# Optimization experiments

Measured on AMD Instinct MI355X. Metric: run time of the kernel, lower is better.

Reference implementation:

```python
import jax, jax.numpy as jnp
import numpy as np
from jax import lax

B, CIN, COUT, H, W, K = 32, 256, 256, 56, 56, 3

def setup_inputs() -> dict:
    key = jax.random.key(0)
    k1, k2, k3 = jax.random.split(key, 3)
    inp = jax.random.normal(k1, (B, CIN, H, W), dtype=jnp.float32)
    # kaiming-style init for conv kernel, normal init for bias
    fan_in = CIN * K * K
    kernel = jax.random.normal(k2, (COUT, CIN, K, K), dtype=jnp.float32) * np.float32(np.sqrt(2.0 / fan_in))
    bias = jax.random.normal(k3, (COUT,), dtype=jnp.float32)
    return {"inp": inp, "kernel": kernel, "bias": bias}

def reference(inp, kernel, bias):
    # Equivalent to the crossbar path: im2col 3x3 patches @ stacked [kernel|bias]
    # matrix == standard conv2d(padding=1, stride=1) + bias.
    out = lax.conv_general_dilated(
        inp, kernel,
        window_strides=(1, 1),
        padding=((1, 1), (1, 1)),
        dimension_numbers=("NCHW", "OIHW", "NCHW"),
    )
    return out + bias[None, :, None, None]
```

## Files before the change

kernel.cpp:

```cpp
#include <hip/hip_runtime.h>
#include <hip/hip_bf16.h>


#define BB   32
#define CINC 256
#define COUTC 256
#define HH   56
#define WW   56
#define HP   58
#define WP   58
#define PIX_PER_IMG (HH*WW)
#define NPIX (BB*PIX_PER_IMG)
#define KTOT (9*CINC)
#define KB_STEPS (KTOT/32)

#define XT_ELEMS ((size_t)BB*HP*WP*CINC)
#define XT_BYTES (XT_ELEMS*2)
#define WR_ELEMS ((size_t)COUTC*KTOT)
#define WR_BYTES (WR_ELEMS*2)

#define BM 128
#define BN 128
#define BK 32

using frag_t = __attribute__((ext_vector_type(8))) short;
using f32x4  = __attribute__((ext_vector_type(4))) float;

__device__ __forceinline__ void gload_lds16(const void* gsrc, void* ldst) {
  __builtin_amdgcn_global_load_lds(
      (const __attribute__((address_space(1))) unsigned*)gsrc,
      (__attribute__((address_space(3))) unsigned*)ldst, 16, 0, 0);
}

__global__ void xpose_kernel(const float* __restrict__ inp,
                             __hip_bfloat16* __restrict__ xt) {
  int bid = blockIdx.x;
  int hp = bid % HP;
  int t  = bid / HP;
  int cb = t % 4;
  int b  = t / 4;
  __shared__ __hip_bfloat16 tile[64 * 60];
  int tid = threadIdx.x;
  for (int i = tid; i < 64 * 60; i += 256) tile[i] = __float2bfloat16(0.f);
  __syncthreads();
  int h = hp - 1;
  if (h >= 0 && h < HH) {
    const float* src = inp + ((size_t)(b * CINC + cb * 64) * HH + h) * WW;
    for (int i = tid; i < 64 * WW; i += 256) {
      int ci = i / WW, w = i - ci * WW;
      tile[ci * 60 + (w + 1)] = __float2bfloat16(src[(size_t)ci * HH * WW + w]);
    }
  }
  __syncthreads();
  __hip_bfloat16* dst = xt + ((size_t)(b * HP + hp) * WP) * CINC + cb * 64;
  for (int i = tid; i < WP * 64; i += 256) {
    int wp = i >> 6, ci = i & 63;
    dst[(size_t)wp * CINC + ci] = tile[ci * 60 + wp];
  }
}

__global__ void wprep_kernel(const float* __restrict__ k4,
                             __hip_bfloat16* __restrict__ wr) {
  int i = blockIdx.x * 256 + threadIdx.x;
  if (i >= (int)WR_ELEMS) return;
  int co = i / KTOT;
  int k  = i - co * KTOT;
  int tap = k >> 8;
  int ci  = k & 255;
  wr[i] = __float2bfloat16(k4[(co * CINC + ci) * 9 + tap]);
}

__global__ void conv_mfma(const __hip_bfloat16* __restrict__ xt,
                          const __hip_bfloat16* __restrict__ wr,
                          const float* __restrict__ bias,
                          float* __restrict__ out) {
  __shared__ alignas(16) __hip_bfloat16 Alds[BM * BK];
  __shared__ alignas(16) __hip_bfloat16 Blds[BN * BK];

  const int tid  = threadIdx.x;
  const int lane = tid & 63;
  const int wid  = tid >> 6;
  const int wrm  = wid >> 1;
  const int wcn  = wid & 1;
  const int ntile = blockIdx.x;
  const int co0   = blockIdx.y * BM;

  const int qa0 = wid * 128 + lane;
  const int qa1 = qa0 + 64;
  const char* wr_b = (const char*)wr;
  const char* xt_b = (const char*)xt;

  const size_t a_src0 = ((size_t)(co0 + (qa0 >> 2)) * KTOT + (qa0 & 3) * 8) * 2;
  const size_t a_src1 = ((size_t)(co0 + (qa1 >> 2)) * KTOT + (qa1 & 3) * 8) * 2;

  int pxg0 = ntile * BN + (qa0 >> 2);
  int pxg1 = ntile * BN + (qa1 >> 2);
  int b0 = pxg0 / PIX_PER_IMG, hw0 = pxg0 - b0 * PIX_PER_IMG;
  int b1 = pxg1 / PIX_PER_IMG, hw1 = pxg1 - b1 * PIX_PER_IMG;
  int h0 = hw0 / WW, w0 = hw0 - h0 * WW;
  int h1 = hw1 / WW, w1 = hw1 - h1 * WW;
  const size_t b_src0 = ((((size_t)b0 * HP + h0) * WP + w0) * CINC + (qa0 & 3) * 8) * 2;
  const size_t b_src1 = ((((size_t)b1 * HP + h1) * WP + w1) * CINC + (qa1 & 3) * 8) * 2;

  char* a_dst0 = (char*)Alds + (wid * 2) * 1024;
  char* a_dst1 = (char*)Alds + (wid * 2 + 1) * 1024;
  char* b_dst0 = (char*)Blds + (wid * 2) * 1024;
  char* b_dst1 = (char*)Blds + (wid * 2 + 1) * 1024;

  f32x4 acc[4][4] = {};

  const int g  = lane >> 4;
  const int fr = lane & 15;

  for (int kb = 0; kb < KB_STEPS; ++kb) {
    int tap = kb >> 3;
    int r = tap / 3;
    int s = tap - r * 3;
    int ci0 = (kb & 7) * 32;
    size_t aoff = (size_t)kb * 64;
    size_t boff = ((size_t)(r * WP + s) * CINC + ci0) * 2;

    __syncthreads();
    gload_lds16(wr_b + a_src0 + aoff, a_dst0);
    gload_lds16(wr_b + a_src1 + aoff, a_dst1);
    gload_lds16(xt_b + b_src0 + boff, b_dst0);
    gload_lds16(xt_b + b_src1 + boff, b_dst1);
    __syncthreads();

    frag_t a[4], bf[4];
#pragma unroll
    for (int m = 0; m < 4; ++m) {
      int row = wrm * 64 + m * 16 + fr;
      a[m] = *(const frag_t*)((const char*)Alds + row * 64 + g * 16);
    }
#pragma unroll
    for (int n = 0; n < 4; ++n) {
      int row = wcn * 64 + n * 16 + fr;
      bf[n] = *(const frag_t*)((const char*)Blds + row * 64 + g * 16);
    }
#pragma unroll
    for (int m = 0; m < 4; ++m)
#pragma unroll
      for (int n = 0; n < 4; ++n)
        acc[m][n] = __builtin_amdgcn_mfma_f32_16x16x32_bf16(a[m], bf[n], acc[m][n], 0, 0, 0);
  }

  const int fq = lane >> 4;
  int pb[4], phw[4];
#pragma unroll
  for (int n = 0; n < 4; ++n) {
    int pxg = ntile * BN + wcn * 64 + n * 16 + fr;
    pb[n]  = pxg / PIX_PER_IMG;
    phw[n] = pxg - pb[n] * PIX_PER_IMG;
  }
#pragma unroll
  for (int m = 0; m < 4; ++m) {
#pragma unroll
    for (int rg = 0; rg < 4; ++rg) {
      int co = co0 + wrm * 64 + m * 16 + fq * 4 + rg;
      float bv = bias[co];
#pragma unroll
      for (int n = 0; n < 4; ++n) {
        out[((size_t)pb[n] * COUTC + co) * PIX_PER_IMG + phw[n]] = acc[m][n][rg] + bv;
      }
    }
  }
}

__global__ void conv_direct(const float* __restrict__ inp,
                            const float* __restrict__ kern,
                            const float* __restrict__ bias,
                            float* __restrict__ out) {
  int idx = blockIdx.x * 256 + threadIdx.x;
  if (idx >= BB * COUTC * PIX_PER_IMG) return;
  int w = idx % WW;
  int t = idx / WW;
  int h = t % HH; t /= HH;
  int co = t % COUTC;
  int b  = t / COUTC;
  float acc = bias[co];
  for (int ci = 0; ci < CINC; ++ci)
    for (int r = 0; r < 3; ++r) {
      int hh = h + r - 1;
      if (hh < 0 || hh >= HH) continue;
      for (int s = 0; s < 3; ++s) {
        int ww2 = w + s - 1;
        if (ww2 < 0 || ww2 >= WW) continue;
        acc += inp[((size_t)(b * CINC + ci) * HH + hh) * WW + ww2] *
               kern[(co * CINC + ci) * 9 + r * 3 + s];
      }
    }
  out[idx] = acc;
}

extern "C" void kernel_launch(void* const* d_in, const int* in_sizes, int n_in,
                              void* d_out, int out_size, void* d_ws, size_t ws_size,
                              hipStream_t stream) {
  const float* inp  = (const float*)d_in[0];
  const float* kern = (const float*)d_in[1];
  const float* bias = (const float*)d_in[2];
  float* out = (float*)d_out;

  size_t need = XT_BYTES + WR_BYTES;
  if (ws_size < need) {
    int tot = BB * COUTC * PIX_PER_IMG;
    conv_direct<<<(tot + 255) / 256, 256, 0, stream>>>(inp, kern, bias, out);
    return;
  }

  __hip_bfloat16* xt  = (__hip_bfloat16*)d_ws;
  __hip_bfloat16* wrp = (__hip_bfloat16*)((char*)d_ws + XT_BYTES);

  xpose_kernel<<<BB * 4 * HP, 256, 0, stream>>>(inp, xt);
  wprep_kernel<<<(int)((WR_ELEMS + 255) / 256), 256, 0, stream>>>(kern, wrp);
  conv_mfma<<<dim3(NPIX / BN, COUTC / BM), 256, 0, stream>>>(xt, wrp, bias, out);
}
```

Baseline: 209.2 us.

## Rewrite conv GEMM with 32x32 MFMA, triple-buffered LDS pipeline and swizzle

Replaces the single-buffered 128x128 implicit-GEMM kernel with a 256-output-channel by 128-pixel tile. It uses 32x32x16 bf16 MFMAs, a three-stage LDS ring buffer filled by async global-to-LDS loads issued two steps ahead, and an XOR swizzle of the LDS chunks. The block index is remapped so neighbouring blocks are spread across the pixel range. The aim is to overlap global loads with MFMA work, halve the redundant input loads caused by the two channel tiles, and cut LDS bank conflicts. In exchange it uses more LDS and accumulator registers per block and depends on hand-placed waitcnt and barrier ordering.

```diff
diff --git a/kernel.cpp b/kernel.cpp
--- a/kernel.cpp
+++ b/kernel.cpp
@@ -2,29 +2,27 @@
 #include <hip/hip_bf16.h>
 
 
-#define BB   32
-#define CINC 256
+#define BB    32
+#define CINC  256
 #define COUTC 256
-#define HH   56
-#define WW   56
-#define HP   58
-#define WP   58
-#define PIX_PER_IMG (HH*WW)
-#define NPIX (BB*PIX_PER_IMG)
-#define KTOT (9*CINC)
-#define KB_STEPS (KTOT/32)
-
-#define XT_ELEMS ((size_t)BB*HP*WP*CINC)
-#define XT_BYTES (XT_ELEMS*2)
+#define HH    56
+#define WW    56
+#define HP    58
+#define WP    58
+#define PIX_PER_IMG 3136
+#define NPIX  100352
+#define KTOT  2304
+#define NKT   72
+
+#define XT_BYTES ((size_t)BB*HP*WP*CINC*2)
 #define WR_ELEMS ((size_t)COUTC*KTOT)
 #define WR_BYTES (WR_ELEMS*2)
 
-#define BM 128
-#define BN 128
-#define BK 32
+#define BUF_SZ 24576
+#define B_OFF  16384
 
 using frag_t = __attribute__((ext_vector_type(8))) short;
-using f32x4  = __attribute__((ext_vector_type(4))) float;
+using f32x16 = __attribute__((ext_vector_type(16))) float;
 
 __device__ __forceinline__ void gload_lds16(const void* gsrc, void* ldst) {
   __builtin_amdgcn_global_load_lds(
@@ -70,99 +68,140 @@
   wr[i] = __float2bfloat16(k4[(co * CINC + ci) * 9 + tap]);
 }
 
-__global__ void conv_mfma(const __hip_bfloat16* __restrict__ xt,
-                          const __hip_bfloat16* __restrict__ wr,
-                          const float* __restrict__ bias,
-                          float* __restrict__ out) {
-  __shared__ alignas(16) __hip_bfloat16 Alds[BM * BK];
-  __shared__ alignas(16) __hip_bfloat16 Blds[BN * BK];
+__global__ __launch_bounds__(256, 2) void conv_mfma32(
+    const __hip_bfloat16* __restrict__ xt,
+    const __hip_bfloat16* __restrict__ wr,
+    const float* __restrict__ bias,
+    float* __restrict__ out) {
+  __shared__ alignas(16) char lds[3 * BUF_SZ];
 
   const int tid  = threadIdx.x;
   const int lane = tid & 63;
   const int wid  = tid >> 6;
-  const int wrm  = wid >> 1;
-  const int wcn  = wid & 1;
-  const int ntile = blockIdx.x;
-  const int co0   = blockIdx.y * BM;
-
-  const int qa0 = wid * 128 + lane;
-  const int qa1 = qa0 + 64;
+  const int wm   = wid >> 1;
+  const int wn   = wid & 1;
+  const int l31  = lane & 31;
+  const int lhi  = lane >> 5;
+
+  const int bid   = blockIdx.x;
+  const int ntile = (bid & 7) * 98 + (bid >> 3);
+
   const char* wr_b = (const char*)wr;
   const char* xt_b = (const char*)xt;
 
-  const size_t a_src0 = ((size_t)(co0 + (qa0 >> 2)) * KTOT + (qa0 & 3) * 8) * 2;
-  const size_t a_src1 = ((size_t)(co0 + (qa1 >> 2)) * KTOT + (qa1 & 3) * 8) * 2;
-
-  int pxg0 = ntile * BN + (qa0 >> 2);
-  int pxg1 = ntile * BN + (qa1 >> 2);
-  int b0 = pxg0 / PIX_PER_IMG, hw0 = pxg0 - b0 * PIX_PER_IMG;
-  int b1 = pxg1 / PIX_PER_IMG, hw1 = pxg1 - b1 * PIX_PER_IMG;
-  int h0 = hw0 / WW, w0 = hw0 - h0 * WW;
-  int h1 = hw1 / WW, w1 = hw1 - h1 * WW;
-  const size_t b_src0 = ((((size_t)b0 * HP + h0) * WP + w0) * CINC + (qa0 & 3) * 8) * 2;
-  const size_t b_src1 = ((((size_t)b1 * HP + h1) * WP + w1) * CINC + (qa1 & 3) * 8) * 2;
-
-  char* a_dst0 = (char*)Alds + (wid * 2) * 1024;
-  char* a_dst1 = (char*)Alds + (wid * 2 + 1) * 1024;
-  char* b_dst0 = (char*)Blds + (wid * 2) * 1024;
-  char* b_dst1 = (char*)Blds + (wid * 2 + 1) * 1024;
-
-  f32x4 acc[4][4] = {};
-
-  const int g  = lane >> 4;
-  const int fr = lane & 15;
-
-  for (int kb = 0; kb < KB_STEPS; ++kb) {
-    int tap = kb >> 3;
-    int r = tap / 3;
-    int s = tap - r * 3;
-    int ci0 = (kb & 7) * 32;
-    size_t aoff = (size_t)kb * 64;
-    size_t boff = ((size_t)(r * WP + s) * CINC + ci0) * 2;
-
-    __syncthreads();
-    gload_lds16(wr_b + a_src0 + aoff, a_dst0);
-    gload_lds16(wr_b + a_src1 + aoff, a_dst1);
-    gload_lds16(xt_b + b_src0 + boff, b_dst0);
-    gload_lds16(xt_b + b_src1 + boff, b_dst1);
-    __syncthreads();
-
-    frag_t a[4], bf[4];
-#pragma unroll
-    for (int m = 0; m < 4; ++m) {
-      int row = wrm * 64 + m * 16 + fr;
-      a[m] = *(const frag_t*)((const char*)Alds + row * 64 + g * 16);
-    }
-#pragma unroll
-    for (int n = 0; n < 4; ++n) {
-      int row = wcn * 64 + n * 16 + fr;
-      bf[n] = *(const frag_t*)((const char*)Blds + row * 64 + g * 16);
-    }
-#pragma unroll
-    for (int m = 0; m < 4; ++m)
-#pragma unroll
-      for (int n = 0; n < 4; ++n)
-        acc[m][n] = __builtin_amdgcn_mfma_f32_16x16x32_bf16(a[m], bf[n], acc[m][n], 0, 0, 0);
-  }
-
-  const int fq = lane >> 4;
-  int pb[4], phw[4];
-#pragma unroll
-  for (int n = 0; n < 4; ++n) {
-    int pxg = ntile * BN + wcn * 64 + n * 16 + fr;
+  const int lr = lane >> 2;
+  const int sc = (((lane & 3) ^ (lr & 3)) << 4);
+
+  const char* pA0 = wr_b + (size_t)(wid * 64 +  0 + lr) * (KTOT * 2) + sc;
+  const char* pA1 = wr_b + (size_t)(wid * 64 + 16 + lr) * (KTOT * 2) + sc;
+  const char* pA2 = wr_b + (size_t)(wid * 64 + 32 + lr) * (KTOT * 2) + sc;
+  const char* pA3 = wr_b + (size_t)(wid * 64 + 48 + lr) * (KTOT * 2) + sc;
+
+  auto mkB = [&](int jb) -> const char* {
+    int px = ntile * 128 + (wid * 2 + jb) * 16 + lr;
+    int b  = px / PIX_PER_IMG;
+    int hw = px - b * PIX_PER_IMG;
+    int h = hw / WW, w = hw - h * WW;
+    return xt_b + (size_t)((b * HP + h) * WP + w) * (CINC * 2) + sc;
+  };
+  const char* pB0 = mkB(0);
+  const char* pB1 = mkB(1);
+
+#define STG_A(WB, T2) {                                                    \
+    size_t _ao = (size_t)(T2) * 64;                                        \
+    gload_lds16(pA0 + _ao, lds + (WB)*BUF_SZ + (wid * 4 + 0) * 1024);      \
+    gload_lds16(pA1 + _ao, lds + (WB)*BUF_SZ + (wid * 4 + 1) * 1024);      \
+    gload_lds16(pA2 + _ao, lds + (WB)*BUF_SZ + (wid * 4 + 2) * 1024); }
+
+#define STG_B(WB, T2) {                                                    \
+    int _tap = (T2) >> 3; int _rr = _tap / 3, _ss = _tap - _rr * 3;        \
+    size_t _ao = (size_t)(T2) * 64;                                        \
+    size_t _bo = (size_t)(_rr * WP + _ss) * (CINC * 2)                     \
+               + (size_t)((T2) & 7) * 64;                                  \
+    gload_lds16(pA3 + _ao, lds + (WB)*BUF_SZ + (wid * 4 + 3) * 1024);      \
+    gload_lds16(pB0 + _bo, lds + (WB)*BUF_SZ + B_OFF + (wid*2+0) * 1024);  \
+    gload_lds16(pB1 + _bo, lds + (WB)*BUF_SZ + B_OFF + (wid*2+1) * 1024); }
+
+  const int aoff  = (wm * 128 + l31) * 64;
+  const int boffr = (wn * 64 + l31) * 64;
+  const int ck0   = ((lhi ^ (l31 & 3)) << 4);
+  const int ck1   = (((2 + lhi) ^ (l31 & 3)) << 4);
+
+  frag_t fa0[4], fb0[2], fa1[4], fb1[2];
+  f32x16 acc[4][2] = {};
+
+#define RSL(RB, CK, FA, FB) {                                              \
+    const char* _b = lds + (RB)*BUF_SZ;                                    \
+    _Pragma("unroll") for (int m = 0; m < 4; ++m)                          \
+      FA[m] = *(const frag_t*)(_b + aoff + m * 2048 + (CK));               \
+    _Pragma("unroll") for (int n = 0; n < 2; ++n)                          \
+      FB[n] = *(const frag_t*)(_b + B_OFF + boffr + n * 2048 + (CK)); }
+
+#define MF(FA, FB) {                                                       \
+    _Pragma("unroll") for (int m = 0; m < 4; ++m)                          \
+    _Pragma("unroll") for (int n = 0; n < 2; ++n)                          \
+      acc[m][n] = __builtin_amdgcn_mfma_f32_32x32x16_bf16(                 \
+          FA[m], FB[n], acc[m][n], 0, 0, 0); }
+
+#define BODY(T, RB, WB, NB) {                                              \
+    RSL(RB, ck1, fa1, fb1);                                                \
+    STG_A(WB, (T) + 2);                                                    \
+    MF(fa0, fb0);                                                          \
+    STG_B(WB, (T) + 2);                                                    \
+    asm volatile("s_waitcnt lgkmcnt(0)" ::: "memory");                     \
+    asm volatile("s_waitcnt vmcnt(6)" ::: "memory");                       \
+    __builtin_amdgcn_s_barrier();                                          \
+    __builtin_amdgcn_sched_barrier(0);                                     \
+    RSL(NB, ck0, fa0, fb0);                                                \
+    MF(fa1, fb1); }
+
+  STG_A(0, 0); STG_B(0, 0);
+  STG_A(1, 1); STG_B(1, 1);
+  asm volatile("s_waitcnt vmcnt(6)" ::: "memory");
+  __builtin_amdgcn_s_barrier();
+  __builtin_amdgcn_sched_barrier(0);
+  RSL(0, ck0, fa0, fb0);
+
+  for (int base = 0; base < 69; base += 3) {
+    BODY(base + 0, 0, 2, 1);
+    BODY(base + 1, 1, 0, 2);
+    BODY(base + 2, 2, 1, 0);
+  }
+  BODY(69, 0, 2, 1);
+
+  {
+    RSL(1, ck1, fa1, fb1);
+    MF(fa0, fb0);
+    asm volatile("s_waitcnt lgkmcnt(0)" ::: "memory");
+    asm volatile("s_waitcnt vmcnt(0)" ::: "memory");
+    __builtin_amdgcn_s_barrier();
+    __builtin_amdgcn_sched_barrier(0);
+    RSL(2, ck0, fa0, fb0);
+    MF(fa1, fb1);
+  }
+  {
+    RSL(2, ck1, fa1, fb1);
+    MF(fa0, fb0);
+    MF(fa1, fb1);
+  }
+
+  int pb[2], phw[2];
+#pragma unroll
+  for (int n = 0; n < 2; ++n) {
+    int pxg = ntile * 128 + wn * 64 + n * 32 + l31;
     pb[n]  = pxg / PIX_PER_IMG;
     phw[n] = pxg - pb[n] * PIX_PER_IMG;
   }
 #pragma unroll
   for (int m = 0; m < 4; ++m) {
 #pragma unroll
-    for (int rg = 0; rg < 4; ++rg) {
-      int co = co0 + wrm * 64 + m * 16 + fq * 4 + rg;
+    for (int r = 0; r < 16; ++r) {
+      int co = wm * 128 + m * 32 + (r & 3) + 8 * (r >> 2) + 4 * lhi;
       float bv = bias[co];
 #pragma unroll
-      for (int n = 0; n < 4; ++n) {
-        out[((size_t)pb[n] * COUTC + co) * PIX_PER_IMG + phw[n]] = acc[m][n][rg] + bv;
-      }
+      for (int n = 0; n < 2; ++n)
+        out[((size_t)pb[n] * COUTC + co) * PIX_PER_IMG + phw[n]] =
+            acc[m][n][r] + bv;
     }
   }
 }
@@ -213,5 +252,5 @@
 
   xpose_kernel<<<BB * 4 * HP, 256, 0, stream>>>(inp, xt);
   wprep_kernel<<<(int)((WR_ELEMS + 255) / 256), 256, 0, stream>>>(kern, wrp);
-  conv_mfma<<<dim3(NPIX / BN, COUTC / BM), 256, 0, stream>>>(xt, wrp, bias, out);
-}
+  conv_mfma32<<<NPIX / 128, 256, 0, stream>>>(xt, wrp, bias, out);
+}
```

Result: faster. 196.6 us (-6.0%).
